# Kernel tuning notes

Measured on AMD Instinct MI355X. Metric: run time of the kernel, lower is better.

## Reference

```python
import jax, jax.numpy as jnp
import numpy as np

HID = 64
STEP = 0.05  # rk4 fixed step; t in [0, 0.2] -> 4 steps
NSTEPS = 4


def setup_inputs() -> dict:
    key = jax.random.key(0)
    ks = jax.random.split(key, 4)
    coords = jax.random.uniform(ks[0], (1, 96, 96, 96, 3), jnp.float32, -1.0, 1.0)

    def mlp_params(k):
        k1, k2 = jax.random.split(k)
        W1 = jax.random.normal(k1, (3, HID), jnp.float32) * 0.3
        b1 = jnp.zeros((HID,), jnp.float32)
        W2 = jax.random.normal(k2, (HID, 3), jnp.float32) * 0.3
        b2 = jnp.zeros((3,), jnp.float32)
        return W1, b1, W2, b2

    W1_0, b1_0, W2_0, b2_0 = mlp_params(ks[1])
    W1_1, b1_1, W2_1, b2_1 = mlp_params(ks[2])
    moving_img = jax.random.uniform(ks[3], (128, 128, 128), jnp.float32)
    return dict(coords=coords,
                W1_0=W1_0, b1_0=b1_0, W2_0=W2_0, b2_0=b2_0,
                W1_1=W1_1, b1_1=b1_1, W2_1=W2_1, b2_1=b2_1,
                moving_img=moving_img)


def _integrate(y, W1, b1, W2, b2):
    """Fixed-step RK4 on dy/dt = f(y) over t in [0, 0.2], step 0.05."""
    f = jax.checkpoint(lambda u: jnp.tanh(u @ W1 + b1) @ W2 + b2)
    h = jnp.float32(STEP)

    def step(y, _):
        k1 = f(y)
        k2 = f(y + 0.5 * h * k1)
        k3 = f(y + 0.5 * h * k2)
        k4 = f(y + h * k3)
        return y + (h / 6.0) * (k1 + 2.0 * k2 + 2.0 * k3 + k4), None

    y, _ = jax.lax.scan(step, y, None, length=NSTEPS)
    return y


def _grid_sample3d(vol, c):
    """torch F.grid_sample 3D, bilinear(trilinear), padding_mode=zeros,
    align_corners=False. c[..., [2,1,0]] reorder from the module means:
    c[...,2] -> x (W axis), c[...,1] -> y (H axis), c[...,0] -> z (D axis)."""
    D, H, W = vol.shape
    x = ((c[..., 2] + 1.0) * W - 1.0) * 0.5
    y = ((c[..., 1] + 1.0) * H - 1.0) * 0.5
    z = ((c[..., 0] + 1.0) * D - 1.0) * 0.5
    x0f, y0f, z0f = jnp.floor(x), jnp.floor(y), jnp.floor(z)
    tx, ty, tz = x - x0f, y - y0f, z - z0f
    x0 = x0f.astype(jnp.int32); x1 = x0 + 1
    y0 = y0f.astype(jnp.int32); y1 = y0 + 1
    z0 = z0f.astype(jnp.int32); z1 = z0 + 1

    def tap(zi, yi, xi, w):
        valid = (zi >= 0) & (zi < D) & (yi >= 0) & (yi < H) & (xi >= 0) & (xi < W)
        v = vol[jnp.clip(zi, 0, D - 1), jnp.clip(yi, 0, H - 1), jnp.clip(xi, 0, W - 1)]
        return jnp.where(valid, v, 0.0) * w

    out = (tap(z0, y0, x0, (1 - tz) * (1 - ty) * (1 - tx)) +
           tap(z0, y0, x1, (1 - tz) * (1 - ty) * tx) +
           tap(z0, y1, x0, (1 - tz) * ty * (1 - tx)) +
           tap(z0, y1, x1, (1 - tz) * ty * tx) +
           tap(z1, y0, x0, tz * (1 - ty) * (1 - tx)) +
           tap(z1, y0, x1, tz * (1 - ty) * tx) +
           tap(z1, y1, x0, tz * ty * (1 - tx)) +
           tap(z1, y1, x1, tz * ty * tx))
    return out


def reference(coords, W1_0, b1_0, W2_0, b2_0, W1_1, b1_1, W2_1, b2_1, moving_img):
    shp = coords.shape                      # [b, h, w, d, 3]
    flat = coords.reshape(-1, 3)            # [N, 3]
    c0 = _integrate(flat, W1_0, b1_0, W2_0, b2_0)          # first ODE warp
    c1 = _integrate(c0, W1_1, b1_1, W2_1, b2_1).reshape(shp)  # second ODE warp
    s = _grid_sample3d(moving_img, c1)      # [b, h, w, d]
    reg_out = (s[..., None] - 0.5) * 2.0    # [b, h, w, d, 1]
    return reg_out, c1
```

## Files before the change

kernel.cpp:

```cpp
#include <hip/hip_runtime.h>
#include <hip/hip_bf16.h>

#define NPTS (96 * 96 * 96)
#define HID 64
#define H_EFF 0.2f

#define TB  49
#define TB2 (TB * TB)
#define TB3 (TB * TB * TB)
#define TB_SCALE 24.0f
#define TB_INV   0.0416666679f
#define QS   8192.0f
#define QSI  (1.0f / 8192.0f)
#define TBL_OFF_B 4128
#define VOLB_OFF_B 945408
#define VOL_N   (128 * 128 * 128)
#define WS_NEED ((size_t)VOLB_OFF_B + (size_t)VOL_N)

#define BUILD_BLOCKS 460
#define CONV_BLOCKS  1024

typedef float v2f __attribute__((ext_vector_type(2)));
typedef float f4  __attribute__((ext_vector_type(4)));
typedef unsigned u2 __attribute__((ext_vector_type(2)));
typedef unsigned u4 __attribute__((ext_vector_type(4)));
typedef short s4v __attribute__((ext_vector_type(4)));

__device__ __forceinline__ float bf2f(const __hip_bfloat16 v) {
    return __bfloat162float(v);
}
__device__ __forceinline__ v2f splat(float x) { v2f r; r.x = x; r.y = x; return r; }
__device__ __forceinline__ v2f vfma(v2f a, v2f b, v2f c) {
    return __builtin_elementwise_fma(a, b, c);
}
__device__ __forceinline__ float lerp1(float a, float b, float f) {
    return __builtin_fmaf(f, b - a, a);
}

__device__ __forceinline__ int bpx(int x) { return ((x >> 3) << 7) | (x & 7); }
__device__ __forceinline__ int bpy(int y) { return ((y >> 2) << 11) | ((y & 3) << 3); }
__device__ __forceinline__ int bpz(int z) { return ((z >> 2) << 16) | ((z & 3) << 5); }

__device__ __forceinline__ int detect_bf16(const void* p, int tid, int* sflag) {
    if (tid < 64) {
        unsigned e = (((const unsigned short*)p)[tid] >> 7) & 0xFFu;
        unsigned long long m = __ballot(e >= 97u && e <= 129u);
        if (tid == 0) *sflag = (__popcll(m) >= 52) ? 1 : 0;
    }
    __syncthreads();
    return *sflag;
}

__global__ void setup_kernel(
    const void* __restrict__ coords,
    const void* __restrict__ W1_0, const void* __restrict__ b1_0,
    const void* __restrict__ W2_0, const void* __restrict__ b2_0,
    const void* __restrict__ W1_1, const void* __restrict__ b1_1,
    const void* __restrict__ W2_1, const void* __restrict__ b2_1,
    const void* __restrict__ vol,
    float* __restrict__ ws) {
    __shared__ int sflags[3];
    int tid = threadIdx.x;
    if (tid < 64) {
        auto sane = [](const void* p, int i) -> bool {
            unsigned e = (((const unsigned short*)p)[i] >> 7) & 0xFFu;
            return e >= 97u && e <= 129u;
        };
        unsigned long long m;
        m = __ballot(sane(W1_0, tid));
        if (tid == 0) sflags[2] = (__popcll(m) >= 52) ? 1 : 0;
        m = __ballot(sane(coords, tid));
        if (tid == 0) sflags[0] = (__popcll(m) >= 52) ? 1 : 0;
        m = __ballot(sane(vol, tid));
        if (tid == 0) sflags[1] = (__popcll(m) >= 52) ? 1 : 0;
    }
    __syncthreads();
    int isbf = sflags[2];
    const float K = 2.88539008177792681472f;
    int ode = tid >> 9;
    int r = tid & 511;
    const void* W1 = ode ? W1_1 : W1_0;
    const void* b1 = ode ? b1_1 : b1_0;
    const void* W2 = ode ? W2_1 : W2_0;
    const void* b2 = ode ? b2_1 : b2_0;
    auto ld = [&](const void* p, int idx) -> float {
        return isbf ? bf2f(((const __hip_bfloat16*)p)[idx]) : ((const float*)p)[idx];
    };
    float v = 0.0f;
    if (r < 192)       v = K * ld(W1, r);
    else if (r < 256)  v = K * ld(b1, r - 192);
    else if (r < 448)  v = -2.0f * ld(W2, r - 256);
    else if (r < 451) {
        int k = r - 448;
        float s = ld(b2, k);
        for (int j = 0; j < HID; ++j) s += ld(W2, 3 * j + k);
        v = s;
    }
    ws[(ode << 9) + r] = v;
    if (tid < 2) ((int*)(ws + 1024))[tid] = sflags[tid];
}

__device__ __forceinline__ void mlp_f2(const float* __restrict__ w,
                                       v2f y0, v2f y1, v2f y2,
                                       v2f& o0, v2f& o1, v2f& o2) {
    v2f a0 = splat(w[448]), a1 = splat(w[449]), a2 = splat(w[450]);
#pragma unroll 8
    for (int j = 0; j < HID; ++j) {
        v2f pre = vfma(y0, splat(w[j]),
                  vfma(y1, splat(w[64 + j]),
                  vfma(y2, splat(w[128 + j]), splat(w[192 + j]))));
        v2f e;
        e.x = __builtin_amdgcn_exp2f(pre.x);
        e.y = __builtin_amdgcn_exp2f(pre.y);
        v2f q = e + splat(1.0f);
        float rP = __builtin_amdgcn_rcpf(q.x * q.y);
        v2f r;
        r.x = q.y * rP;
        r.y = q.x * rP;
        a0 = vfma(r, splat(w[256 + 3 * j + 0]), a0);
        a1 = vfma(r, splat(w[256 + 3 * j + 1]), a1);
        a2 = vfma(r, splat(w[256 + 3 * j + 2]), a2);
    }
    o0 = a0; o1 = a1; o2 = a2;
}

__device__ __forceinline__ void integrate2(const float* __restrict__ ws,
                                           v2f& y0, v2f& y1, v2f& y2) {
    const float h = H_EFF;
#pragma unroll 1
    for (int ode = 0; ode < 2; ++ode) {
        const float* __restrict__ w = ws + (ode << 9);
        v2f k0 = splat(0.f), k1 = splat(0.f), k2 = splat(0.f);
        v2f s0 = splat(0.f), s1 = splat(0.f), s2 = splat(0.f);
#pragma unroll 1
        for (int e = 0; e < 4; ++e) {
            float ae = (e == 0) ? 0.0f : ((e == 3) ? h : 0.5f * h);
            float we = (e == 1 || e == 2) ? 2.0f : 1.0f;
            v2f aev = splat(ae), wev = splat(we);
            v2f f0, f1, f2;
            mlp_f2(w, vfma(aev, k0, y0), vfma(aev, k1, y1), vfma(aev, k2, y2),
                   f0, f1, f2);
            k0 = f0; k1 = f1; k2 = f2;
            s0 = vfma(wev, k0, s0);
            s1 = vfma(wev, k1, s1);
            s2 = vfma(wev, k2, s2);
        }
        v2f h6 = splat(h / 6.0f);
        y0 = vfma(h6, s0, y0);
        y1 = vfma(h6, s1, y1);
        y2 = vfma(h6, s2, y2);
    }
}

__global__ __launch_bounds__(256) void prep_kernel(
    const void* __restrict__ W1_0, const void* __restrict__ b1_0,
    const void* __restrict__ W2_0, const void* __restrict__ b2_0,
    const void* __restrict__ W1_1, const void* __restrict__ b1_1,
    const void* __restrict__ W2_1, const void* __restrict__ b2_1,
    const void* __restrict__ vol,
    float* __restrict__ ws) {
    int tid = threadIdx.x;
    if (blockIdx.x < BUILD_BLOCKS) {
        __shared__ int sflag;
        __shared__ f4 sw1[2][64];
        __shared__ f4 sw2[2][64];
        __shared__ float sb2[2][4];
        int isbf = detect_bf16(W1_0, tid, &sflag);
        const float K = 2.88539008177792681472f;
        auto ld = [&](const void* p, int idx) -> float {
            return isbf ? bf2f(((const __hip_bfloat16*)p)[idx]) : ((const float*)p)[idx];
        };
        {
            int ode = (tid >> 6) & 1;
            int j = tid & 63;
            const void* W1 = ode ? W1_1 : W1_0;
            const void* b1 = ode ? b1_1 : b1_0;
            const void* W2 = ode ? W2_1 : W2_0;
            if (tid < 128) {
                f4 c = { K * ld(W1, j), K * ld(W1, 64 + j),
                         K * ld(W1, 128 + j), K * ld(b1, j) };
                sw1[ode][j] = c;
            } else {
                f4 c = { -2.f * ld(W2, 3 * j + 0), -2.f * ld(W2, 3 * j + 1),
                         -2.f * ld(W2, 3 * j + 2), 0.f };
                sw2[ode][j] = c;
            }
            if (tid < 6) {
                int o = tid / 3, k = tid - 3 * o;
                const void* W2o = o ? W2_1 : W2_0;
                const void* b2o = o ? b2_1 : b2_0;
                float s = ld(b2o, k);
                for (int jj = 0; jj < HID; ++jj) s += ld(W2o, 3 * jj + k);
                sb2[o][k] = s;
            }
        }
        __syncthreads();

        int gtid = blockIdx.x * 256 + tid;
        int lp = gtid >> 1;
        int h  = gtid & 1;
        int nA = 2 * lp;
        if (nA >= TB3) return;
        int nB = nA + 1;
        int nBc = nB < TB3 ? nB : (TB3 - 1);

        auto node_y = [](int n, float* a, float* b, float* c) {
            int i0 = n / TB2;
            int rem = n - i0 * TB2;
            int i1 = rem / TB;
            int i2 = rem - i1 * TB;
            *a = __builtin_fmaf((float)i0, TB_INV, -1.0f);
            *b = __builtin_fmaf((float)i1, TB_INV, -1.0f);
            *c = __builtin_fmaf((float)i2, TB_INV, -1.0f);
        };
        float ax, bx, cxv, ay, by, cyv;
        node_y(nA,  &ax, &bx, &cxv);
        node_y(nBc, &ay, &by, &cyv);
        v2f y0, y1, y2;
        y0.x = ax;  y1.x = bx;  y2.x = cxv;
        y0.y = ay;  y1.y = by;  y2.y = cyv;

        const float hh = H_EFF;
        int jbase = h << 5;
#pragma unroll 1
        for (int ode = 0; ode < 2; ++ode) {
            const f4* __restrict__ w1 = sw1[ode];
            const f4* __restrict__ w2 = sw2[ode];
            v2f b2v0 = h ? splat(0.f) : splat(sb2[ode][0]);
            v2f b2v1 = h ? splat(0.f) : splat(sb2[ode][1]);
            v2f b2v2 = h ? splat(0.f) : splat(sb2[ode][2]);
            v2f k0 = splat(0.f), k1 = splat(0.f), k2 = splat(0.f);
            v2f s0 = splat(0.f), s1 = splat(0.f), s2 = splat(0.f);
#pragma unroll 1
            for (int e = 0; e < 4; ++e) {
                float ae = (e == 0) ? 0.0f : ((e == 3) ? hh : 0.5f * hh);
                float we = (e == 1 || e == 2) ? 2.0f : 1.0f;
                v2f aev = splat(ae), wev = splat(we);
                v2f z0 = vfma(aev, k0, y0);
                v2f z1 = vfma(aev, k1, y1);
                v2f z2 = vfma(aev, k2, y2);
                v2f a0 = b2v0, a1 = b2v1, a2 = b2v2;
#pragma unroll 8
                for (int jj = 0; jj < 32; ++jj) {
                    f4 c1 = w1[jbase + jj];
                    v2f pre = vfma(z0, splat(c1.x),
                              vfma(z1, splat(c1.y),
                              vfma(z2, splat(c1.z), splat(c1.w))));
                    v2f ev;
                    ev.x = __builtin_amdgcn_exp2f(pre.x);
                    ev.y = __builtin_amdgcn_exp2f(pre.y);
                    v2f q = ev + splat(1.0f);
                    float rP = __builtin_amdgcn_rcpf(q.x * q.y);
                    v2f r;
                    r.x = q.y * rP;
                    r.y = q.x * rP;
                    f4 c2 = w2[jbase + jj];
                    a0 = vfma(r, splat(c2.x), a0);
                    a1 = vfma(r, splat(c2.y), a1);
                    a2 = vfma(r, splat(c2.z), a2);
                }
                v2f t;
                t.x = __shfl_xor(a0.x, 1); t.y = __shfl_xor(a0.y, 1); a0 += t;
                t.x = __shfl_xor(a1.x, 1); t.y = __shfl_xor(a1.y, 1); a1 += t;
                t.x = __shfl_xor(a2.x, 1); t.y = __shfl_xor(a2.y, 1); a2 += t;
                k0 = a0; k1 = a1; k2 = a2;
                s0 = vfma(wev, k0, s0);
                s1 = vfma(wev, k1, s1);
                s2 = vfma(wev, k2, s2);
            }
            v2f h6 = splat(hh / 6.0f);
            y0 = vfma(h6, s0, y0);
            y1 = vfma(h6, s1, y1);
            y2 = vfma(h6, s2, y2);
        }

        if (h == 0) {
            auto quant = [](float v) -> short {
                float q = v * QS;
                q = q < -32767.f ? -32767.f : (q > 32767.f ? 32767.f : q);
                return (short)(int)rintf(q);
            };
            s4v* T = (s4v*)((char*)ws + TBL_OFF_B);
            s4v qA = { quant(y0.x), quant(y1.x), quant(y2.x), 0 };
            T[nA] = qA;
            if (nB < TB3) {
                s4v qB = { quant(y0.y), quant(y1.y), quant(y2.y), 0 };
                T[nB] = qB;
            }
        }
    } else {
        __shared__ int svf;
        int vbf = detect_bf16(vol, tid, &svf);
        int g = (blockIdx.x - BUILD_BLOCKS) * 256 + tid;
        int d0 = g * 8;
        int x0 = ((d0 >> 7) & 15) << 3;
        int yy = (((d0 >> 11) & 31) << 2) | ((d0 >> 3) & 3);
        int zz = (((d0 >> 16) & 31) << 2) | ((d0 >> 5) & 3);
        int src = (zz << 14) | (yy << 7) | x0;
        float v[8];
        if (vbf) {
            u4 w = *(const u4*)((const unsigned short*)vol + src);
#pragma unroll
            for (int i = 0; i < 4; ++i) {
                unsigned ww = w[i];
                v[2 * i + 0] = __builtin_bit_cast(float, ww << 16);
                v[2 * i + 1] = __builtin_bit_cast(float, ww & 0xFFFF0000u);
            }
        } else {
            const f4* F = (const f4*)((const float*)vol + src);
            f4 A = F[0], B = F[1];
            v[0] = A.x; v[1] = A.y; v[2] = A.z; v[3] = A.w;
            v[4] = B.x; v[5] = B.y; v[6] = B.z; v[7] = B.w;
        }
        unsigned q[8];
#pragma unroll
        for (int i = 0; i < 8; ++i) {
            float qq = __builtin_fmaf(v[i], 255.0f, 0.5f);
            qq = qq < 0.f ? 0.f : (qq > 255.f ? 255.f : qq);
            q[i] = (unsigned)qq;
        }
        u2 pk;
        pk.x = q[0] | (q[1] << 8) | (q[2] << 16) | (q[3] << 24);
        pk.y = q[4] | (q[5] << 8) | (q[6] << 16) | (q[7] << 24);
        *(u2*)((unsigned char*)ws + VOLB_OFF_B + d0) = pk;
    }
}

__device__ __forceinline__ float sample3d(const void* __restrict__ vol, int vbf,
                                          float cz, float cy, float cx) {
    float fx = (cx + 1.0f) * 64.0f - 0.5f;
    float fy = (cy + 1.0f) * 64.0f - 0.5f;
    float fz = (cz + 1.0f) * 64.0f - 0.5f;
    float x0f = floorf(fx), y0f = floorf(fy), z0f = floorf(fz);
    float tx = fx - x0f, ty = fy - y0f, tz = fz - z0f;
    int x0 = (int)x0f, y0 = (int)y0f, z0 = (int)z0f;
    int x1 = x0 + 1, y1 = y0 + 1, z1 = z0 + 1;
    auto clampi = [](int v) { return v < 0 ? 0 : (v > 127 ? 127 : v); };
    auto valid = [](int zi, int yi, int xi) -> bool {
        return ((unsigned)zi < 128u) && ((unsigned)yi < 128u) && ((unsigned)xi < 128u);
    };
    int xc0 = clampi(x0), xc1 = clampi(x1);
    int yc0 = clampi(y0), yc1 = clampi(y1);
    int zc0 = clampi(z0), zc1 = clampi(z1);
    int idx[8] = {
        (zc0 << 14) | (yc0 << 7) | xc0, (zc0 << 14) | (yc0 << 7) | xc1,
        (zc0 << 14) | (yc1 << 7) | xc0, (zc0 << 14) | (yc1 << 7) | xc1,
        (zc1 << 14) | (yc0 << 7) | xc0, (zc1 << 14) | (yc0 << 7) | xc1,
        (zc1 << 14) | (yc1 << 7) | xc0, (zc1 << 14) | (yc1 << 7) | xc1 };
    float v[8];
    if (vbf) {
        const __hip_bfloat16* V = (const __hip_bfloat16*)vol;
#pragma unroll
        for (int q = 0; q < 8; ++q) v[q] = bf2f(V[idx[q]]);
    } else {
        const float* V = (const float*)vol;
#pragma unroll
        for (int q = 0; q < 8; ++q) v[q] = V[idx[q]];
    }
    if (!valid(z0, y0, x0)) v[0] = 0.f;
    if (!valid(z0, y0, x1)) v[1] = 0.f;
    if (!valid(z0, y1, x0)) v[2] = 0.f;
    if (!valid(z0, y1, x1)) v[3] = 0.f;
    if (!valid(z1, y0, x0)) v[4] = 0.f;
    if (!valid(z1, y0, x1)) v[5] = 0.f;
    if (!valid(z1, y1, x0)) v[6] = 0.f;
    if (!valid(z1, y1, x1)) v[7] = 0.f;
    return v[0] * (1.f - tz) * (1.f - ty) * (1.f - tx) +
           v[1] * (1.f - tz) * (1.f - ty) * tx +
           v[2] * (1.f - tz) * ty * (1.f - tx) +
           v[3] * (1.f - tz) * ty * tx +
           v[4] * tz * (1.f - ty) * (1.f - tx) +
           v[5] * tz * (1.f - ty) * tx +
           v[6] * tz * ty * (1.f - tx) +
           v[7] * tz * ty * tx;
}

__global__ __launch_bounds__(256) void query_kernel(
    const void* __restrict__ coords,
    const float* __restrict__ ws,
    float* __restrict__ out) {
    __shared__ int scf;
    int cbf = detect_bf16(coords, threadIdx.x, &scf);
    int t = blockIdx.x * 256 + threadIdx.x;
    if (t >= NPTS / 4) return;

    float y[4][3];
    if (cbf) {
        const u2* C2 = (const u2*)((const unsigned short*)coords + 12 * t);
        u2 ua = __builtin_nontemporal_load(C2);
        u2 ub = __builtin_nontemporal_load(C2 + 1);
        u2 uc = __builtin_nontemporal_load(C2 + 2);
        unsigned uu[6] = {ua.x, ua.y, ub.x, ub.y, uc.x, uc.y};
#pragma unroll
        for (int p = 0; p < 4; ++p)
#pragma unroll
            for (int d = 0; d < 3; ++d) {
                int k = 3 * p + d;
                unsigned h = uu[k >> 1];
                h = (k & 1) ? (h & 0xFFFF0000u) : (h << 16);
                y[p][d] = __builtin_bit_cast(float, h);
            }
    } else {
        const f4* C4 = (const f4*)((const float*)coords + 12 * t);
        f4 a = __builtin_nontemporal_load(C4);
        f4 b = __builtin_nontemporal_load(C4 + 1);
        f4 c = __builtin_nontemporal_load(C4 + 2);
        y[0][0] = a.x; y[0][1] = a.y; y[0][2] = a.z;
        y[1][0] = a.w; y[1][1] = b.x; y[1][2] = b.y;
        y[2][0] = b.z; y[2][1] = b.w; y[2][2] = c.x;
        y[3][0] = c.y; y[3][1] = c.z; y[3][2] = c.w;
    }

    auto cell = [](float tt, int* idx, float* f) {
        int v = (int)floorf(tt);
        v = v < 0 ? 0 : (v > TB - 2 ? TB - 2 : v);
        *idx = v; *f = tt - (float)v;
    };

    int bidx[4];
    float ff[4][3];
#pragma unroll
    for (int p = 0; p < 4; ++p) {
        float t0 = (y[p][0] + 1.0f) * TB_SCALE;
        float t1 = (y[p][1] + 1.0f) * TB_SCALE;
        float t2 = (y[p][2] + 1.0f) * TB_SCALE;
        int i0, i1, i2;
        cell(t0, &i0, &ff[p][0]);
        cell(t1, &i1, &ff[p][1]);
        cell(t2, &i2, &ff[p][2]);
        bidx[p] = (i0 * TB + i1) * TB + i2;
    }

    const s4v* T = (const s4v*)((const char*)ws + TBL_OFF_B);
    s4v ev[4][8];
#pragma unroll
    for (int p = 0; p < 4; ++p) {
        int b = bidx[p];
        ev[p][0] = T[b];                 ev[p][1] = T[b + 1];
        ev[p][2] = T[b + TB];            ev[p][3] = T[b + TB + 1];
        ev[p][4] = T[b + TB2];           ev[p][5] = T[b + TB2 + 1];
        ev[p][6] = T[b + TB2 + TB];      ev[p][7] = T[b + TB2 + TB + 1];
    }

    float c1v[4][3];
#pragma unroll
    for (int p = 0; p < 4; ++p) {
        float f0 = ff[p][0], f1 = ff[p][1], f2 = ff[p][2];
#pragma unroll
        for (int d = 0; d < 3; ++d) {
            float a00 = lerp1((float)ev[p][0][d], (float)ev[p][1][d], f2);
            float a01 = lerp1((float)ev[p][2][d], (float)ev[p][3][d], f2);
            float a10 = lerp1((float)ev[p][4][d], (float)ev[p][5][d], f2);
            float a11 = lerp1((float)ev[p][6][d], (float)ev[p][7][d], f2);
            c1v[p][d] = lerp1(lerp1(a00, a01, f1), lerp1(a10, a11, f1), f0) * QSI;
        }
    }

    {
        float* dst = out + NPTS + 12 * t;
        f4 s0 = {c1v[0][0], c1v[0][1], c1v[0][2], c1v[1][0]};
        f4 s1 = {c1v[1][1], c1v[1][2], c1v[2][0], c1v[2][1]};
        f4 s2 = {c1v[2][2], c1v[3][0], c1v[3][1], c1v[3][2]};
        ((f4*)dst)[0] = s0;
        ((f4*)dst)[1] = s1;
        ((f4*)dst)[2] = s2;
    }

    const unsigned char* VB = (const unsigned char*)ws + VOLB_OFF_B;
    f4 o;
#pragma unroll
    for (int p = 0; p < 4; ++p) {
        float fx = (c1v[p][2] + 1.0f) * 64.0f - 0.5f;
        float fy = (c1v[p][1] + 1.0f) * 64.0f - 0.5f;
        float fz = (c1v[p][0] + 1.0f) * 64.0f - 0.5f;
        float x0f = floorf(fx), y0f = floorf(fy), z0f = floorf(fz);
        float tx = fx - x0f, ty = fy - y0f, tz = fz - z0f;
        int x0 = (int)x0f, y0 = (int)y0f, z0 = (int)z0f;
        int x1 = x0 + 1, y1 = y0 + 1, z1 = z0 + 1;
        auto clampi = [](int v) { return v < 0 ? 0 : (v > 127 ? 127 : v); };
        auto valid = [](int zi, int yi, int xi) -> bool {
            return ((unsigned)zi < 128u) && ((unsigned)yi < 128u) &&
                   ((unsigned)xi < 128u);
        };
        int px0 = bpx(clampi(x0)), px1 = bpx(clampi(x1));
        int py0 = bpy(clampi(y0)), py1 = bpy(clampi(y1));
        int pz0 = bpz(clampi(z0)), pz1 = bpz(clampi(z1));
        float v[8];
        v[0] = (float)VB[pz0 | py0 | px0];
        v[1] = (float)VB[pz0 | py0 | px1];
        v[2] = (float)VB[pz0 | py1 | px0];
        v[3] = (float)VB[pz0 | py1 | px1];
        v[4] = (float)VB[pz1 | py0 | px0];
        v[5] = (float)VB[pz1 | py0 | px1];
        v[6] = (float)VB[pz1 | py1 | px0];
        v[7] = (float)VB[pz1 | py1 | px1];
        if (!valid(z0, y0, x0)) v[0] = 0.f;
        if (!valid(z0, y0, x1)) v[1] = 0.f;
        if (!valid(z0, y1, x0)) v[2] = 0.f;
        if (!valid(z0, y1, x1)) v[3] = 0.f;
        if (!valid(z1, y0, x0)) v[4] = 0.f;
        if (!valid(z1, y0, x1)) v[5] = 0.f;
        if (!valid(z1, y1, x0)) v[6] = 0.f;
        if (!valid(z1, y1, x1)) v[7] = 0.f;
        float sraw =
            v[0] * (1.f - tz) * (1.f - ty) * (1.f - tx) +
            v[1] * (1.f - tz) * (1.f - ty) * tx +
            v[2] * (1.f - tz) * ty * (1.f - tx) +
            v[3] * (1.f - tz) * ty * tx +
            v[4] * tz * (1.f - ty) * (1.f - tx) +
            v[5] * tz * (1.f - ty) * tx +
            v[6] * tz * ty * (1.f - tx) +
            v[7] * tz * ty * tx;
        o[p] = __builtin_fmaf(sraw, 2.0f / 255.0f, -1.0f);
    }
    ((f4*)(out + 4 * t))[0] = o;
}

__global__ __launch_bounds__(64) void diffeo_kernel(
    const void* __restrict__ coords,
    const float* __restrict__ ws,
    const void* __restrict__ vol,
    float* __restrict__ out) {
    int t = blockIdx.x * 64 + threadIdx.x;
    if (t >= NPTS / 2) return;

    const int* flags = (const int*)(ws + 1024);
    int cbf = flags[0];
    int vbf = flags[1];

    v2f y0, y1, y2;
    if (cbf) {
        const __hip_bfloat16* C = (const __hip_bfloat16*)coords;
        int b = 6 * t;
        y0.x = bf2f(C[b + 0]); y1.x = bf2f(C[b + 1]); y2.x = bf2f(C[b + 2]);
        y0.y = bf2f(C[b + 3]); y1.y = bf2f(C[b + 4]); y2.y = bf2f(C[b + 5]);
    } else {
        const float* C = (const float*)coords;
        int b = 6 * t;
        y0.x = C[b + 0]; y1.x = C[b + 1]; y2.x = C[b + 2];
        y0.y = C[b + 3]; y1.y = C[b + 4]; y2.y = C[b + 5];
    }

    integrate2(ws, y0, y1, y2);

    int b = 6 * t;
    out[NPTS + b + 0] = y0.x; out[NPTS + b + 1] = y1.x; out[NPTS + b + 2] = y2.x;
    out[NPTS + b + 3] = y0.y; out[NPTS + b + 4] = y1.y; out[NPTS + b + 5] = y2.y;

    float sA = sample3d(vol, vbf, y0.x, y1.x, y2.x);
    float sB = sample3d(vol, vbf, y0.y, y1.y, y2.y);
    out[2 * t + 0] = __builtin_fmaf(2.0f, sA, -1.0f);
    out[2 * t + 1] = __builtin_fmaf(2.0f, sB, -1.0f);
}

extern "C" void kernel_launch(void* const* d_in, const int* in_sizes, int n_in,
                              void* d_out, int out_size, void* d_ws, size_t ws_size,
                              hipStream_t stream) {
    const void* coords = d_in[0];
    const void* W1_0 = d_in[1];
    const void* b1_0 = d_in[2];
    const void* W2_0 = d_in[3];
    const void* b2_0 = d_in[4];
    const void* W1_1 = d_in[5];
    const void* b1_1 = d_in[6];
    const void* W2_1 = d_in[7];
    const void* b2_1 = d_in[8];
    const void* vol  = d_in[9];
    float* out = (float*)d_out;
    float* ws = (float*)d_ws;

    if (ws_size >= WS_NEED) {
        prep_kernel<<<BUILD_BLOCKS + CONV_BLOCKS, 256, 0, stream>>>(
            W1_0, b1_0, W2_0, b2_0, W1_1, b1_1, W2_1, b2_1, vol, ws);
        query_kernel<<<NPTS / 1024, 256, 0, stream>>>(coords, ws, out);
    } else {
        setup_kernel<<<1, 1024, 0, stream>>>(coords, W1_0, b1_0, W2_0, b2_0,
                                             W1_1, b1_1, W2_1, b2_1, vol, ws);
        diffeo_kernel<<<(NPTS / 2) / 64, 64, 0, stream>>>(coords, ws, vol, out);
    }
}
```

Baseline: 147.3 us.

## Brick the flow lookup table and split table build across four lanes

The precomputed 49^3 displacement table is stored in a bricked layout (2x2x4 blocks), so the eight corner fetches of a trilinear lookup fall into fewer cache lines. The table build now splits each node's 64 hidden units across four lanes instead of two, doubling the build block count and adding an extra shuffle-reduction stage. The workspace offset grows to fit the padded bricked table. Index arithmetic per lookup becomes more complex.

```diff
diff --git a/kernel.cpp b/kernel.cpp
--- a/kernel.cpp
+++ b/kernel.cpp
@@ -13,11 +13,12 @@
 #define QS   8192.0f
 #define QSI  (1.0f / 8192.0f)
 #define TBL_OFF_B 4128
-#define VOLB_OFF_B 945408
+#define TBL_BRICK_BYTES 1040000
+#define VOLB_OFF_B 1044480
 #define VOL_N   (128 * 128 * 128)
 #define WS_NEED ((size_t)VOLB_OFF_B + (size_t)VOL_N)
 
-#define BUILD_BLOCKS 460
+#define BUILD_BLOCKS 920
 #define CONV_BLOCKS  1024
 
 typedef float v2f __attribute__((ext_vector_type(2)));
@@ -40,6 +41,10 @@
 __device__ __forceinline__ int bpx(int x) { return ((x >> 3) << 7) | (x & 7); }
 __device__ __forceinline__ int bpy(int y) { return ((y >> 2) << 11) | ((y & 3) << 3); }
 __device__ __forceinline__ int bpz(int z) { return ((z >> 2) << 16) | ((z & 3) << 5); }
+
+__device__ __forceinline__ int tf0(int i0) { return (i0 >> 1) * 5200 + (i0 & 1) * 8; }
+__device__ __forceinline__ int tf1(int i1) { return (i1 >> 1) * 208 + (i1 & 1) * 4; }
+__device__ __forceinline__ int tf2(int i2) { return (i2 >> 2) * 16 + (i2 & 3); }
 
 __device__ __forceinline__ int detect_bf16(const void* p, int tid, int* sflag) {
     if (tid < 64) {
@@ -197,31 +202,32 @@
         __syncthreads();
 
         int gtid = blockIdx.x * 256 + tid;
-        int lp = gtid >> 1;
-        int h  = gtid & 1;
+        int lp = gtid >> 2;
+        int h  = gtid & 3;
         int nA = 2 * lp;
         if (nA >= TB3) return;
         int nB = nA + 1;
         int nBc = nB < TB3 ? nB : (TB3 - 1);
 
-        auto node_y = [](int n, float* a, float* b, float* c) {
-            int i0 = n / TB2;
-            int rem = n - i0 * TB2;
-            int i1 = rem / TB;
-            int i2 = rem - i1 * TB;
-            *a = __builtin_fmaf((float)i0, TB_INV, -1.0f);
-            *b = __builtin_fmaf((float)i1, TB_INV, -1.0f);
-            *c = __builtin_fmaf((float)i2, TB_INV, -1.0f);
+        auto node_idx = [](int n, int* i0, int* i1, int* i2) {
+            *i0 = n / TB2;
+            int rem = n - *i0 * TB2;
+            *i1 = rem / TB;
+            *i2 = rem - *i1 * TB;
         };
-        float ax, bx, cxv, ay, by, cyv;
-        node_y(nA,  &ax, &bx, &cxv);
-        node_y(nBc, &ay, &by, &cyv);
+        int iA0, iA1, iA2, iB0, iB1, iB2;
+        node_idx(nA,  &iA0, &iA1, &iA2);
+        node_idx(nBc, &iB0, &iB1, &iB2);
         v2f y0, y1, y2;
-        y0.x = ax;  y1.x = bx;  y2.x = cxv;
-        y0.y = ay;  y1.y = by;  y2.y = cyv;
+        y0.x = __builtin_fmaf((float)iA0, TB_INV, -1.0f);
+        y1.x = __builtin_fmaf((float)iA1, TB_INV, -1.0f);
+        y2.x = __builtin_fmaf((float)iA2, TB_INV, -1.0f);
+        y0.y = __builtin_fmaf((float)iB0, TB_INV, -1.0f);
+        y1.y = __builtin_fmaf((float)iB1, TB_INV, -1.0f);
+        y2.y = __builtin_fmaf((float)iB2, TB_INV, -1.0f);
 
         const float hh = H_EFF;
-        int jbase = h << 5;
+        int jbase = h << 4;
 #pragma unroll 1
         for (int ode = 0; ode < 2; ++ode) {
             const f4* __restrict__ w1 = sw1[ode];
@@ -241,7 +247,7 @@
                 v2f z2 = vfma(aev, k2, y2);
                 v2f a0 = b2v0, a1 = b2v1, a2 = b2v2;
 #pragma unroll 8
-                for (int jj = 0; jj < 32; ++jj) {
+                for (int jj = 0; jj < 16; ++jj) {
                     f4 c1 = w1[jbase + jj];
                     v2f pre = vfma(z0, splat(c1.x),
                               vfma(z1, splat(c1.y),
@@ -263,6 +269,9 @@
                 t.x = __shfl_xor(a0.x, 1); t.y = __shfl_xor(a0.y, 1); a0 += t;
                 t.x = __shfl_xor(a1.x, 1); t.y = __shfl_xor(a1.y, 1); a1 += t;
                 t.x = __shfl_xor(a2.x, 1); t.y = __shfl_xor(a2.y, 1); a2 += t;
+                t.x = __shfl_xor(a0.x, 2); t.y = __shfl_xor(a0.y, 2); a0 += t;
+                t.x = __shfl_xor(a1.x, 2); t.y = __shfl_xor(a1.y, 2); a1 += t;
+                t.x = __shfl_xor(a2.x, 2); t.y = __shfl_xor(a2.y, 2); a2 += t;
                 k0 = a0; k1 = a1; k2 = a2;
                 s0 = vfma(wev, k0, s0);
                 s1 = vfma(wev, k1, s1);
@@ -282,10 +291,10 @@
             };
             s4v* T = (s4v*)((char*)ws + TBL_OFF_B);
             s4v qA = { quant(y0.x), quant(y1.x), quant(y2.x), 0 };
-            T[nA] = qA;
+            T[tf0(iA0) + tf1(iA1) + tf2(iA2)] = qA;
             if (nB < TB3) {
                 s4v qB = { quant(y0.y), quant(y1.y), quant(y2.y), 0 };
-                T[nB] = qB;
+                T[tf0(iB0) + tf1(iB1) + tf2(iB2)] = qB;
             }
         }
     } else {
@@ -417,29 +426,33 @@
         *idx = v; *f = tt - (float)v;
     };
 
-    int bidx[4];
+    int ia[4][3];
     float ff[4][3];
 #pragma unroll
     for (int p = 0; p < 4; ++p) {
         float t0 = (y[p][0] + 1.0f) * TB_SCALE;
         float t1 = (y[p][1] + 1.0f) * TB_SCALE;
         float t2 = (y[p][2] + 1.0f) * TB_SCALE;
-        int i0, i1, i2;
-        cell(t0, &i0, &ff[p][0]);
-        cell(t1, &i1, &ff[p][1]);
-        cell(t2, &i2, &ff[p][2]);
-        bidx[p] = (i0 * TB + i1) * TB + i2;
+        cell(t0, &ia[p][0], &ff[p][0]);
+        cell(t1, &ia[p][1], &ff[p][1]);
+        cell(t2, &ia[p][2], &ff[p][2]);
     }
 
     const s4v* T = (const s4v*)((const char*)ws + TBL_OFF_B);
     s4v ev[4][8];
 #pragma unroll
     for (int p = 0; p < 4; ++p) {
-        int b = bidx[p];
-        ev[p][0] = T[b];                 ev[p][1] = T[b + 1];
-        ev[p][2] = T[b + TB];            ev[p][3] = T[b + TB + 1];
-        ev[p][4] = T[b + TB2];           ev[p][5] = T[b + TB2 + 1];
-        ev[p][6] = T[b + TB2 + TB];      ev[p][7] = T[b + TB2 + TB + 1];
+        int a0 = tf0(ia[p][0]), a0b = tf0(ia[p][0] + 1);
+        int a1 = tf1(ia[p][1]), a1b = tf1(ia[p][1] + 1);
+        int a2 = tf2(ia[p][2]), a2b = tf2(ia[p][2] + 1);
+        ev[p][0] = T[a0 + a1 + a2];
+        ev[p][1] = T[a0 + a1 + a2b];
+        ev[p][2] = T[a0 + a1b + a2];
+        ev[p][3] = T[a0 + a1b + a2b];
+        ev[p][4] = T[a0b + a1 + a2];
+        ev[p][5] = T[a0b + a1 + a2b];
+        ev[p][6] = T[a0b + a1b + a2];
+        ev[p][7] = T[a0b + a1b + a2b];
     }
 
     float c1v[4][3];
```

Measured after the change: 174.4 us. +18.4%, slower.
